# Kernel tuning notes

Hardware: AMD Instinct MI355X
Metric: run time of the kernel (lower is better)

Reference implementation:

```python
import jax, jax.numpy as jnp
import numpy as np

EPS = 1e-5

def layernorm(x, g, b):
    mu = jnp.mean(x, axis=-1, keepdims=True)
    var = jnp.var(x, axis=-1, keepdims=True)
    return (x - mu) * jax.lax.rsqrt(var + EPS) * g + b

def setup_inputs() -> dict:
    B, S, H = 8, 2048, 1024
    key = jax.random.key(0)
    ks = jax.random.split(key, 8)
    lim = 1.0 / np.sqrt(2 * H)  # torch Linear default init scale
    return {
        "input_states": jax.random.normal(ks[0], (B, S, H), jnp.float32),
        "in_g": jnp.ones((H,), jnp.float32), "in_b": jnp.zeros((H,), jnp.float32),
        "st_g": jnp.ones((H,), jnp.float32), "st_b": jnp.zeros((H,), jnp.float32),
        "Wu": jax.random.uniform(ks[1], (H, 2 * H), jnp.float32, -lim, lim),
        "bu": jax.random.uniform(ks[2], (H,), jnp.float32, -lim, lim),
        "Wr": jax.random.uniform(ks[3], (H, 2 * H), jnp.float32, -lim, lim),
        "br": jax.random.uniform(ks[4], (H,), jnp.float32, -lim, lim),
        "Wo": jax.random.uniform(ks[5], (H, 2 * H), jnp.float32, -lim, lim),
        "bo": jax.random.uniform(ks[6], (H,), jnp.float32, -lim, lim),
        "ln_g": jnp.ones((H,), jnp.float32), "ln_b": jnp.zeros((H,), jnp.float32),
    }

def reference(input_states, in_g, in_b, st_g, st_b, Wu, bu, Wr, br, Wo, bo, ln_g, ln_b):
    B, S, H = input_states.shape
    xn = layernorm(input_states, in_g, in_b)            # [B,S,H]
    h0 = jnp.zeros((B, H), input_states.dtype)
    nh0 = layernorm(h0, st_g, st_b)                     # = st_b (zeros input)

    def step(carry, x_t):
        h, nh = carry
        comb = jnp.concatenate([x_t, nh], axis=-1)      # [B,2H]
        u = jax.nn.sigmoid(comb @ Wu.T + bu)
        r = jax.nn.sigmoid(comb @ Wr.T + br)
        comb2 = jnp.concatenate([x_t, r * nh], axis=-1)
        c = jnp.tanh(comb2 @ Wo.T + bo)
        h = (1.0 - u) * h + u * c
        nh = layernorm(h, st_g, st_b)
        return (h, nh), h                               # dropout is identity (eval)

    _, hs = jax.lax.scan(step, (h0, nh0), jnp.swapaxes(xn, 0, 1))  # hs: [S,B,H]
    outputs = jnp.swapaxes(hs, 0, 1)                    # [B,S,H]
    return layernorm(outputs, ln_g, ln_b)
```

## Files before the change

### kernel.cpp

```cpp
#include <hip/hip_runtime.h>


typedef unsigned short bf16_t;
typedef unsigned int u32_t;
typedef u32_t u32x2 __attribute__((ext_vector_type(2)));
typedef u32_t u32x4 __attribute__((ext_vector_type(4)));

__device__ __forceinline__ float bf2f(bf16_t u) {
    return __uint_as_float(((unsigned)u) << 16);
}
__device__ __forceinline__ float bf2f_hi(u32_t d) {
    return __uint_as_float(d & 0xFFFF0000u);
}
__device__ __forceinline__ float bf2f_lo(u32_t d) {
    return __uint_as_float(d << 16);
}
__device__ __forceinline__ bf16_t f2bf(float f) {
    unsigned u = __float_as_uint(f);
    unsigned r = (u + 0x7FFFu + ((u >> 16) & 1u)) >> 16;
    return (bf16_t)r;
}

#define B_  8
#define S_  2048
#define H_  1024
#define EPS 1e-5f
#define NB  512
#define NT  512
#define SENT 0xFFFFu
#define GUARD_MAX 3000000L

template<bool SC1>
__device__ __forceinline__ void tstore(u32_t* p, u32_t v) {
    if (SC1) asm volatile("global_store_dword %0, %1, off sc0 sc1" :: "v"(p), "v"(v) : "memory");
    else     asm volatile("global_store_dword %0, %1, off"          :: "v"(p), "v"(v) : "memory");
}
template<bool SC1>
__device__ __forceinline__ void tstore4(u32_t* p, u32x4 v) {
    if (SC1) asm volatile("global_store_dwordx4 %0, %1, off sc0 sc1" :: "v"(p), "v"(v) : "memory");
    else     asm volatile("global_store_dwordx4 %0, %1, off"          :: "v"(p), "v"(v) : "memory");
}
template<bool SC1>
__device__ __forceinline__ void tload2(u32x2& v, const u32_t* p) {
    if (SC1) asm volatile("global_load_dwordx2 %0, %1, off sc0 sc1" : "=v"(v) : "v"(p));
    else     asm volatile("global_load_dwordx2 %0, %1, off sc0"     : "=v"(v) : "v"(p));
}
template<bool SC1>
__device__ __forceinline__ void tload4(u32x4& v, const u32_t* p) {
    if (SC1) asm volatile("global_load_dwordx4 %0, %1, off sc0 sc1" : "=v"(v) : "v"(p));
    else     asm volatile("global_load_dwordx4 %0, %1, off sc0"     : "=v"(v) : "v"(p));
}
template<bool SC1>
__device__ __forceinline__ u32x2 poll2(const u32_t* p, u32_t tag, long& guard) {
    u32x2 v;
    if (guard > GUARD_MAX) {
        tload2<SC1>(v, p);
        asm volatile("s_waitcnt vmcnt(0)" ::: "memory");
        return v;
    }
    for (;;) {
        tload2<SC1>(v, p);
        asm volatile("s_waitcnt vmcnt(0)" ::: "memory");
        __builtin_amdgcn_sched_barrier(0);
        if ((((v.x ^ tag) | (v.y ^ tag)) & 0xFFFFu) == 0) break;
        __builtin_amdgcn_s_sleep(1);
        if (++guard > GUARD_MAX) break;
    }
    return v;
}

__device__ __forceinline__ float dotp8(u32x4 W, u32x4 X) {
    return bf2f_lo(W.x) * bf2f_lo(X.x) + bf2f_hi(W.x) * bf2f_hi(X.x)
         + bf2f_lo(W.y) * bf2f_lo(X.y) + bf2f_hi(W.y) * bf2f_hi(X.y)
         + bf2f_lo(W.z) * bf2f_lo(X.z) + bf2f_hi(W.z) * bf2f_hi(X.z)
         + bf2f_lo(W.w) * bf2f_lo(X.w) + bf2f_hi(W.w) * bf2f_hi(X.w);
}

__device__ __forceinline__ int rdv(u32_t* cnt, unsigned need, int tid, int* sdead) {
    __syncthreads();
    if (tid == 0) {
        __hip_atomic_fetch_add(cnt, 1u, __ATOMIC_ACQ_REL, __HIP_MEMORY_SCOPE_AGENT);
        long g = 0;
        while (__hip_atomic_load(cnt, __ATOMIC_ACQUIRE, __HIP_MEMORY_SCOPE_AGENT) < need) {
            __builtin_amdgcn_s_sleep(2);
            if (++g > 5000000L) { *sdead = 1; break; }
        }
    }
    __syncthreads();
    return *sdead;
}

__global__ void detect_flag(const unsigned* __restrict__ in_g_bits, int* flag,
                            u32_t* __restrict__ epoch) {
    *flag = (in_g_bits[0] == 0x3F800000u) ? 0 : 1;
    *epoch = *epoch + 1u;
}

__global__ __launch_bounds__(256) void canon_vec(
    const void* v0, const void* v1, const void* v2, const void* v3,
    const void* v4, const void* v5, const void* v6, const void* v7,
    const void* v8, float* __restrict__ dst, const int* __restrict__ flagp)
{
    int isbf = *flagp;
    const void* srcs[9] = {v0, v1, v2, v3, v4, v5, v6, v7, v8};
    const void* s = srcs[blockIdx.y];
    int k = blockIdx.x * 256 + threadIdx.x;
    float val = isbf ? bf2f(((const bf16_t*)s)[k]) : ((const float*)s)[k];
    dst[(long)blockIdx.y * H_ + k] = val;
}

__global__ __launch_bounds__(256) void canon_wh(
    const void* Wu, const void* Wr, const void* Wo,
    bf16_t* __restrict__ Whu, bf16_t* __restrict__ Whr, bf16_t* __restrict__ Who,
    const int* __restrict__ flagp)
{
    int isbf = *flagp;
    const void* srcs[3] = {Wu, Wr, Wo};
    bf16_t* dsts[3] = {Whu, Whr, Who};
    const void* s = srcs[blockIdx.y];
    bf16_t* d = dsts[blockIdx.y];
    long j = blockIdx.x;
#pragma unroll
    for (int i = 0; i < 4; i++) {
        int k = threadIdx.x + i * 256;
        long off = j * (2 * H_) + H_ + k;
        bf16_t v = isbf ? ((const bf16_t*)s)[off] : f2bf(((const float*)s)[off]);
        d[j * H_ + k] = v;
    }
}

__global__ __launch_bounds__(256) void ln_in(
    const void* __restrict__ src, const float* __restrict__ g,
    const float* __restrict__ bt, bf16_t* __restrict__ dst,
    const int* __restrict__ flagp)
{
    int isbf = *flagp;
    long row = blockIdx.x;
    float v[4];
    float s = 0.f, q = 0.f;
#pragma unroll
    for (int i = 0; i < 4; i++) {
        long idx = row * H_ + threadIdx.x + i * 256;
        v[i] = isbf ? bf2f(((const bf16_t*)src)[idx]) : ((const float*)src)[idx];
        s += v[i];
        q += v[i] * v[i];
    }
#pragma unroll
    for (int off = 32; off; off >>= 1) {
        s += __shfl_down(s, off);
        q += __shfl_down(q, off);
    }
    __shared__ float ls[4], lq[4];
    __shared__ float smu, sri;
    int wid = threadIdx.x >> 6, lane = threadIdx.x & 63;
    if (lane == 0) { ls[wid] = s; lq[wid] = q; }
    __syncthreads();
    if (threadIdx.x == 0) {
        float S = ls[0] + ls[1] + ls[2] + ls[3];
        float Q = lq[0] + lq[1] + lq[2] + lq[3];
        float mu = S * (1.f / H_);
        smu = mu;
        sri = rsqrtf(Q * (1.f / H_) - mu * mu + EPS);
    }
    __syncthreads();
    float mu = smu, ri = sri;
#pragma unroll
    for (int i = 0; i < 4; i++) {
        int k = threadIdx.x + i * 256;
        dst[row * H_ + k] = f2bf((v[i] - mu) * ri * g[k] + bt[k]);
    }
}

__global__ __launch_bounds__(256) void ln_out(
    void* __restrict__ buf, const float* __restrict__ g,
    const float* __restrict__ bt, const int* __restrict__ flagp)
{
    int isbf = *flagp;
    long row = blockIdx.x;
    float v[4];
    float s = 0.f, q = 0.f;
#pragma unroll
    for (int i = 0; i < 4; i++) {
        long idx = row * H_ + threadIdx.x + i * 256;
        v[i] = isbf ? bf2f(((const bf16_t*)buf)[idx]) : ((const float*)buf)[idx];
        s += v[i];
        q += v[i] * v[i];
    }
#pragma unroll
    for (int off = 32; off; off >>= 1) {
        s += __shfl_down(s, off);
        q += __shfl_down(q, off);
    }
    __shared__ float ls[4], lq[4];
    __shared__ float smu, sri;
    int wid = threadIdx.x >> 6, lane = threadIdx.x & 63;
    if (lane == 0) { ls[wid] = s; lq[wid] = q; }
    __syncthreads();
    if (threadIdx.x == 0) {
        float S = ls[0] + ls[1] + ls[2] + ls[3];
        float Q = lq[0] + lq[1] + lq[2] + lq[3];
        float mu = S * (1.f / H_);
        smu = mu;
        sri = rsqrtf(Q * (1.f / H_) - mu * mu + EPS);
    }
    __syncthreads();
    float mu = smu, ri = sri;
#pragma unroll
    for (int i = 0; i < 4; i++) {
        long idx = row * H_ + threadIdx.x + i * 256;
        int k = threadIdx.x + i * 256;
        float o = (v[i] - mu) * ri * g[k] + bt[k];
        if (isbf) ((bf16_t*)buf)[idx] = f2bf(o);
        else      ((float*)buf)[idx] = o;
    }
}

__global__ __launch_bounds__(256) void gemm_pre(
    const bf16_t* __restrict__ A,
    const void* __restrict__ Wu, const void* __restrict__ Wr, const void* __restrict__ Wo,
    const float* __restrict__ bias3,
    bf16_t* __restrict__ Pu, bf16_t* __restrict__ Pr, bf16_t* __restrict__ Po,
    const int* __restrict__ flagp)
{
    int isbf = *flagp;
    const void* W;
    const float* bias = bias3 + (long)blockIdx.z * H_;
    bf16_t* C;
    if (blockIdx.z == 0)      { W = Wu; C = Pu; }
    else if (blockIdx.z == 1) { W = Wr; C = Pr; }
    else                      { W = Wo; C = Po; }

    __shared__ float sa[8][128];
    __shared__ float sb[8][128];
    float acc[8][8];
#pragma unroll
    for (int i = 0; i < 8; i++)
#pragma unroll
        for (int j = 0; j < 8; j++) acc[i][j] = 0.f;

    int tx = threadIdx.x % 16, ty = threadIdx.x / 16;
    int m0 = blockIdx.x * 128, n0 = blockIdx.y * 128;
    int lr = threadIdx.x >> 1;
    int lc = (threadIdx.x & 1) * 4;

    for (int kt = 0; kt < H_; kt += 8) {
        ushort4 av = *(const ushort4*)(A + (long)(m0 + lr) * H_ + kt + lc);
        float w0, w1, w2, w3;
        long woff = (long)(n0 + lr) * (2 * H_) + kt + lc;
        if (isbf) {
            ushort4 bv = *(const ushort4*)((const bf16_t*)W + woff);
            w0 = bf2f(bv.x); w1 = bf2f(bv.y); w2 = bf2f(bv.z); w3 = bf2f(bv.w);
        } else {
            float4 bv = *(const float4*)((const float*)W + woff);
            w0 = bv.x; w1 = bv.y; w2 = bv.z; w3 = bv.w;
        }
        sa[lc + 0][lr] = bf2f(av.x); sa[lc + 1][lr] = bf2f(av.y);
        sa[lc + 2][lr] = bf2f(av.z); sa[lc + 3][lr] = bf2f(av.w);
        sb[lc + 0][lr] = w0; sb[lc + 1][lr] = w1;
        sb[lc + 2][lr] = w2; sb[lc + 3][lr] = w3;
        __syncthreads();
#pragma unroll
        for (int k = 0; k < 8; k++) {
            float ar[8], brg[8];
#pragma unroll
            for (int i = 0; i < 8; i++) ar[i] = sa[k][ty * 8 + i];
#pragma unroll
            for (int j = 0; j < 8; j++) brg[j] = sb[k][tx * 8 + j];
#pragma unroll
            for (int i = 0; i < 8; i++)
#pragma unroll
                for (int j = 0; j < 8; j++) acc[i][j] += ar[i] * brg[j];
        }
        __syncthreads();
    }
#pragma unroll
    for (int i = 0; i < 8; i++) {
        long m = m0 + ty * 8 + i;
#pragma unroll
        for (int j = 0; j < 8; j++) {
            int n = n0 + tx * 8 + j;
            C[m * H_ + n] = f2bf(acc[i][j] + bias[n]);
        }
    }
}

template<bool SC1>
__device__ __forceinline__ void scan_loop(
    int b, int j0, int tid, int isbf,
    const bf16_t* __restrict__ Whu, const bf16_t* __restrict__ Whr,
    const bf16_t* __restrict__ Who,
    const bf16_t* __restrict__ Pu, const bf16_t* __restrict__ Pr,
    const bf16_t* __restrict__ Po,
    u32_t* __restrict__ h_tagb, u32_t* __restrict__ rnh_tagb,
    void* __restrict__ outv,
    const float* __restrict__ g_s, const float* __restrict__ bta_s,
    u32_t* __restrict__ hb_s, float* __restrict__ u_s,
    float* __restrict__ ls, float* __restrict__ lq,
    u32_t* __restrict__ rnst, u32_t* __restrict__ hst)
{
    const int w = tid >> 6, l = tid & 63;

    const int dotA  = w * 8 + (l >> 3);
    const int pA    = l & 7;
    const int gate  = dotA >> 5;
    const int colLA = dotA & 31;
    const int colA  = j0 + colLA;
    const bf16_t* WA = gate ? Whr : Whu;
    const bf16_t* PA = gate ? Pr : Pu;
    u32x4 wa[16];
    {
        const u32x4* src = (const u32x4*)(WA + (long)colA * H_ + pA * 128);
#pragma unroll
        for (int i = 0; i < 16; i++) wa[i] = src[i];
    }
    float cb = 0.f, swg = 0.f;
#pragma unroll
    for (int i = 0; i < 16; i++) {
        u32x4 W = wa[i];
        u32_t nw0, nw1, nw2, nw3;
#pragma unroll
        for (int q = 0; q < 4; q++) {
            int k = pA * 128 + i * 8 + q * 2;
            u32_t wq = (q == 0) ? W.x : (q == 1) ? W.y : (q == 2) ? W.z : W.w;
            float w0 = bf2f_lo(wq), w1 = bf2f_hi(wq);
            cb += w0 * bta_s[k] + w1 * bta_s[k + 1];
            bf16_t f0 = f2bf(w0 * g_s[k]);
            bf16_t f1 = f2bf(w1 * g_s[k + 1]);
            swg += bf2f(f0) + bf2f(f1);
            u32_t packed = (u32_t)f0 | ((u32_t)f1 << 16);
            if (q == 0) nw0 = packed; else if (q == 1) nw1 = packed;
            else if (q == 2) nw2 = packed; else nw3 = packed;
        }
        wa[i].x = nw0; wa[i].y = nw1; wa[i].z = nw2; wa[i].w = nw3;
    }
#pragma unroll
    for (int off = 1; off <= 4; off <<= 1) {
        cb  += __shfl_xor(cb, off);
        swg += __shfl_xor(swg, off);
    }

    const int colLB = w * 4 + (l >> 4);
    const int colB  = j0 + colLB;
    const int oB    = l & 15;
    u32x4 wb[8];
    {
        const u32x4* src = (const u32x4*)(Who + (long)colB * H_ + oB * 64);
#pragma unroll
        for (int i = 0; i < 8; i++) wb[i] = src[i];
    }

    const bool ldrA = (pA == 0);
    const bool ldrB = (oB == 0);
    const u32_t* h_pollp  = h_tagb + tid * 2;
    const u32_t* rn_pollp = rnh_tagb + tid * 2;
    const int hoff = w * 68 + (tid & 63);

    float h_reg = 0.f;
    long guard = 0;

    for (int t = 0; t < S_; t++) {
        float pvalA = 0.f, povalB = 0.f;
        if (ldrA) pvalA = bf2f(PA[((long)b * S_ + t) * H_ + colA]);
        if (ldrB) povalB = bf2f(Po[((long)b * S_ + t) * H_ + colB]);

        float x0, x1;
        u32_t hpk;
        if (t == 0) { x0 = 0.f; x1 = 0.f; hpk = 0u; }
        else {
            u32x2 hv = poll2<SC1>(h_pollp, (u32_t)t, guard);
            x0 = bf2f_hi(hv.x); x1 = bf2f_hi(hv.y);
            hpk = (hv.x >> 16) | (hv.y & 0xFFFF0000u);
        }
        hb_s[hoff] = hpk;
        float s = x0 + x1, q = x0 * x0 + x1 * x1;
#pragma unroll
        for (int off = 32; off; off >>= 1) {
            s += __shfl_xor(s, off);
            q += __shfl_xor(q, off);
        }
        if (l == 0) { ls[w] = s; lq[w] = q; }
        __syncthreads();

        float da = 0.f;
        {
            const u32_t* nb = hb_s + pA * 68;
#pragma unroll
            for (int i = 0; i < 16; i++)
                da += dotp8(wa[i], *(const u32x4*)(nb + i * 4));
        }
#pragma unroll
        for (int off = 1; off <= 4; off <<= 1) da += __shfl_xor(da, off);
        if (ldrA) {
            float S = 0.f, Q = 0.f;
#pragma unroll
            for (int i = 0; i < 8; i++) { S += ls[i]; Q += lq[i]; }
            float mu = S * (1.f / H_);
            float ri = rsqrtf(Q * (1.f / H_) - mu * mu + EPS);
            float acc = ri * (da - mu * swg) + cb;
            float sg = 1.f / (1.f + __expf(-(pvalA + acc)));
            if (gate == 0) {
                u_s[colLA] = sg;
            } else {
                u32_t d = hb_s[(colA >> 7) * 68 + ((colA >> 1) & 63)];
                float hj = (colA & 1) ? bf2f_hi(d) : bf2f_lo(d);
                float nhj = (hj - mu) * ri * g_s[colA] + bta_s[colA];
                rnst[colLA] = ((u32_t)f2bf(sg * nhj) << 16) | (u32_t)(t + 1);
            }
        }
        __syncthreads();
        if (tid < 8)
            tstore4<SC1>(rnh_tagb + j0 + tid * 4, *(const u32x4*)(rnst + tid * 4));

        {
            u32x2 rv = poll2<SC1>(rn_pollp, (u32_t)(t + 1), guard);
            hb_s[hoff] = (rv.x >> 16) | (rv.y & 0xFFFF0000u);
        }
        __syncthreads();

        float db = 0.f;
        {
            const u32_t* nb = hb_s + (oB >> 1) * 68 + (oB & 1) * 32;
#pragma unroll
            for (int i = 0; i < 8; i++)
                db += dotp8(wb[i], *(const u32x4*)(nb + i * 4));
        }
#pragma unroll
        for (int off = 1; off <= 8; off <<= 1) db += __shfl_xor(db, off);
        if (ldrB) {
            float c = tanhf(povalB + db);
            float u = u_s[colLB];
            h_reg = h_reg + u * (c - h_reg);
            hst[colLB] = ((u32_t)f2bf(h_reg) << 16) | (u32_t)(t + 1);
            long op = ((long)b * S_ + t) * H_ + colB;
            if (isbf) ((bf16_t*)outv)[op] = f2bf(h_reg);
            else      ((float*)outv)[op]  = h_reg;
        }
        __syncthreads();
        if (tid < 8)
            tstore4<SC1>(h_tagb + j0 + tid * 4, *(const u32x4*)(hst + tid * 4));
    }
}

__global__ __launch_bounds__(NT, 2) void scan_persist(
    const bf16_t* __restrict__ Whu, const bf16_t* __restrict__ Whr,
    const bf16_t* __restrict__ Who,
    const float* __restrict__ st_g, const float* __restrict__ st_b,
    const bf16_t* __restrict__ Pu, const bf16_t* __restrict__ Pr,
    const bf16_t* __restrict__ Po,
    u32_t* __restrict__ h_tag, u32_t* __restrict__ rnh_tag,
    void* __restrict__ outv, const int* __restrict__ flagp,
    const u32_t* __restrict__ epochp,
    u32_t* __restrict__ probe, u32_t* __restrict__ slots,
    u32_t* __restrict__ cnt1, u32_t* __restrict__ cnt2,
    u32_t* __restrict__ slowf)
{
    __shared__ float g_s[H_], bta_s[H_];
    __shared__ u32_t hb_s[8 * 68];
    __shared__ u32_t rnst[32], hst[32];
    __shared__ float u_s[32];
    __shared__ float ls[8], lq[8];
    __shared__ int s_dead, s_tok, s_bad, s_fast, s_batch, s_slot;

    const int tid = threadIdx.x;
    const int isbf = *flagp;
    const u32_t ep = *epochp;
    const u32_t ep2 = ep ^ 0xA5A50000u;
    u32_t* probe2 = probe + 4096;

    __threadfence();

    if (tid == 0) {
        s_dead = 0; s_tok = 0; s_bad = 0; s_fast = 0;
        int x;
        asm volatile("s_getreg_b32 %0, hwreg(HW_REG_XCC_ID)" : "=s"(x));
        x &= 7;
        int batch = -1, slot = 0;
        unsigned s = atomicAdd(&slots[x], 1u);
        if (s < 32u) { batch = x; slot = (int)s; }
        else {
            for (int wt = 0; wt < 40; wt++) __builtin_amdgcn_s_sleep(127);
            for (int k = 1; k <= 8 && batch < 0; k++) {
                int b2 = (x + k) & 7;
                if (__hip_atomic_load(&slots[b2], __ATOMIC_RELAXED,
                                      __HIP_MEMORY_SCOPE_AGENT) < 32u) {
                    unsigned s2 = atomicAdd(&slots[b2], 1u);
                    if (s2 < 32u) { batch = b2; slot = (int)s2; }
                }
            }
        }
        s_batch = batch; s_slot = slot;
    }
    __syncthreads();
    if (s_batch < 0) return;
    const int b = s_batch, j0 = s_slot * 32, slot = s_slot;
    u32_t* h_tagb   = h_tag   + (long)b * H_;
    u32_t* rnh_tagb = rnh_tag + (long)b * H_;

    for (int i = tid; i < H_; i += NT) { g_s[i] = st_g[i]; bta_s[i] = st_b[i]; }

    if (tid < 32) {
        tstore<true>(h_tagb   + j0 + tid, SENT);
        tstore<true>(rnh_tagb + j0 + tid, SENT);
    }
    asm volatile("s_waitcnt vmcnt(0)" ::: "memory");

    if (rdv(cnt1 + b, 32u, tid, &s_dead)) return;

    {
        if (tid == 0) {
            tstore<false>(probe + ((long)b * 32 + slot) * 16, ep);
            asm volatile("s_waitcnt vmcnt(0)" ::: "memory");
        }
        __syncthreads();
        if (tid < 64) {
            const u32_t* pp = probe + ((long)b * 32 + (tid & 31)) * 16;
            bool ok = false;
            long it = 0;
            for (;;) {
                u32_t v;
                asm volatile("global_load_dword %0, %1, off sc0" : "=v"(v) : "v"(pp));
                asm volatile("s_waitcnt vmcnt(0)" ::: "memory");
                __builtin_amdgcn_sched_barrier(0);
                ok = (tid >= 32) || (v == ep);
                if (__ballot(ok) == ~0ull) break;
                __builtin_amdgcn_s_sleep(2);
                if (++it > 20000L) break;
            }
            if (tid == 0) s_tok = (__ballot(ok) == ~0ull) ? 1 : 0;
        }
        __syncthreads();
        if (s_tok) {
            if (tid == 0) {
                tstore<false>(probe2 + ((long)b * 32 + slot) * 16, ep2);
                asm volatile("s_waitcnt vmcnt(0)" ::: "memory");
            }
            __syncthreads();
            if (tid < 64) {
                const u32_t* pp = probe2 + ((long)b * 32 + (tid & 31)) * 16;
                bool ok = false;
                long it = 0;
                for (;;) {
                    u32_t v;
                    asm volatile("global_load_dword %0, %1, off sc0" : "=v"(v) : "v"(pp));
                    asm volatile("s_waitcnt vmcnt(0)" ::: "memory");
                    __builtin_amdgcn_sched_barrier(0);
                    ok = (tid >= 32) || (v == ep2);
                    if (__ballot(ok) == ~0ull) break;
                    __builtin_amdgcn_s_sleep(2);
                    if (++it > 20000L) break;
                }
                if (tid == 0 && __ballot(ok) != ~0ull) s_tok = 0;
            }
        }
    }
    __syncthreads();

    if (s_tok) {
        const u32_t* sp = (tid < 256) ? (h_tagb + tid * 4)
                                      : (rnh_tagb + (tid - 256) * 4);
        u32x4 a;
        tload4<false>(a, sp);
        asm volatile("s_waitcnt vmcnt(0)" ::: "memory");
        __builtin_amdgcn_sched_barrier(0);
        if (a.x != SENT || a.y != SENT || a.z != SENT || a.w != SENT)
            s_bad = 1;
    }
    __syncthreads();

    if (tid == 0) {
        int fastwant = s_tok && !s_bad;
        if (!fastwant)
            __hip_atomic_fetch_add(slowf + b, 1u, __ATOMIC_ACQ_REL,
                                   __HIP_MEMORY_SCOPE_AGENT);
    }
    if (rdv(cnt2 + b, 32u, tid, &s_dead)) return;
    if (tid == 0)
        s_fast = (__hip_atomic_load(slowf + b, __ATOMIC_ACQUIRE,
                                    __HIP_MEMORY_SCOPE_AGENT) == 0u) ? 1 : 0;
    __syncthreads();

    if (s_fast)
        scan_loop<false>(b, j0, tid, isbf, Whu, Whr, Who, Pu, Pr, Po,
                         h_tagb, rnh_tagb, outv, g_s, bta_s, hb_s, u_s,
                         ls, lq, rnst, hst);
    else
        scan_loop<true>(b, j0, tid, isbf, Whu, Whr, Who, Pu, Pr, Po,
                        h_tagb, rnh_tagb, outv, g_s, bta_s, hb_s, u_s,
                        ls, lq, rnst, hst);
}

extern "C" void kernel_launch(void* const* d_in, const int* in_sizes, int n_in,
                              void* d_out, int out_size, void* d_ws, size_t ws_size,
                              hipStream_t stream)
{
    const void* input = d_in[0];
    const void* in_g  = d_in[1];
    const void* in_b  = d_in[2];
    const void* st_g  = d_in[3];
    const void* st_b  = d_in[4];
    const void* Wu    = d_in[5];
    const void* bu    = d_in[6];
    const void* Wr    = d_in[7];
    const void* br    = d_in[8];
    const void* Wo    = d_in[9];
    const void* bo    = d_in[10];
    const void* ln_g  = d_in[11];
    const void* ln_b  = d_in[12];

    const long NTOK = (long)B_ * S_ * H_;

    char* base = (char*)d_ws;
    int*    flag    = (int*)base;
    u32_t*  epoch   = (u32_t*)(base + 64);
    u32_t*  cnt1    = (u32_t*)(base + 512);
    u32_t*  cnt2    = (u32_t*)(base + 640);
    u32_t*  slowf   = (u32_t*)(base + 768);
    u32_t*  slots   = (u32_t*)(base + 896);
    u32_t*  h_tag   = (u32_t*)(base + 4096);
    u32_t*  rnh_tag = h_tag + (long)B_ * H_;
    float*  vecs    = (float*)(rnh_tag + (long)B_ * H_);
    float* c_stg   = vecs + 0 * H_;
    float* c_stb   = vecs + 1 * H_;
    float* c_ing   = vecs + 2 * H_;
    float* c_inb   = vecs + 3 * H_;
    float* c_lng   = vecs + 4 * H_;
    float* c_lnb   = vecs + 5 * H_;
    float* c_bias3 = vecs + 6 * H_;
    bf16_t* Whu = (bf16_t*)(vecs + 9 * H_);
    bf16_t* Whr = Whu + (long)H_ * H_;
    bf16_t* Who = Whr + (long)H_ * H_;
    bf16_t* Pu  = Who + (long)H_ * H_;
    bf16_t* Pr  = Pu + NTOK;
    bf16_t* Po  = Pr + NTOK;
    u32_t*  probe  = (u32_t*)(Po + NTOK);

    bf16_t* xn = (bf16_t*)d_out;

    detect_flag<<<1, 1, 0, stream>>>((const unsigned*)in_g, flag, epoch);

    canon_vec<<<dim3(H_ / 256, 9), 256, 0, stream>>>(
        st_g, st_b, in_g, in_b, ln_g, ln_b, bu, br, bo, vecs, flag);
    canon_wh<<<dim3(H_, 3), 256, 0, stream>>>(Wu, Wr, Wo, Whu, Whr, Who, flag);

    hipMemsetAsync(base + 128, 0, 4096 - 128, stream);

    ln_in<<<B_ * S_, 256, 0, stream>>>(input, c_ing, c_inb, xn, flag);

    gemm_pre<<<dim3(128, 8, 3), 256, 0, stream>>>(
        xn, Wu, Wr, Wo, c_bias3, Pu, Pr, Po, flag);

    scan_persist<<<NB, NT, 0, stream>>>(
        Whu, Whr, Who, c_stg, c_stb, Pu, Pr, Po,
        h_tag, rnh_tag, d_out, flag, epoch, probe, slots, cnt1, cnt2, slowf);

    ln_out<<<B_ * S_, 256, 0, stream>>>(d_out, c_lng, c_lnb, flag);
}
```

Measured before the change: 12.20 ms.

## Publish tagged scan values directly per lane and spread blocks one-per-CU

In the persistent scan, each leader lane now writes its tagged r*nh and h values straight to global memory. Before, these went into shared staging buffers and were flushed as vector stores after a barrier, so the change shortens the critical path of each sequential step. Block-to-batch assignment also claims one CU per XCC through a CAS-owned table, so that two scan blocks of one batch do not share a CU. Timeout guards are lowered. The trade-off is more, smaller global stores per step and an extra memset.

```diff
diff --git a/kernel.cpp b/kernel.cpp
--- a/kernel.cpp
+++ b/kernel.cpp
@@ -28,17 +28,12 @@
 #define NB  512
 #define NT  512
 #define SENT 0xFFFFu
-#define GUARD_MAX 3000000L
+#define GUARD_MAX 2000000L
 
 template<bool SC1>
 __device__ __forceinline__ void tstore(u32_t* p, u32_t v) {
     if (SC1) asm volatile("global_store_dword %0, %1, off sc0 sc1" :: "v"(p), "v"(v) : "memory");
     else     asm volatile("global_store_dword %0, %1, off"          :: "v"(p), "v"(v) : "memory");
-}
-template<bool SC1>
-__device__ __forceinline__ void tstore4(u32_t* p, u32x4 v) {
-    if (SC1) asm volatile("global_store_dwordx4 %0, %1, off sc0 sc1" :: "v"(p), "v"(v) : "memory");
-    else     asm volatile("global_store_dwordx4 %0, %1, off"          :: "v"(p), "v"(v) : "memory");
 }
 template<bool SC1>
 __device__ __forceinline__ void tload2(u32x2& v, const u32_t* p) {
@@ -83,7 +78,7 @@
         long g = 0;
         while (__hip_atomic_load(cnt, __ATOMIC_ACQUIRE, __HIP_MEMORY_SCOPE_AGENT) < need) {
             __builtin_amdgcn_s_sleep(2);
-            if (++g > 5000000L) { *sdead = 1; break; }
+            if (++g > 3000000L) { *sdead = 1; break; }
         }
     }
     __syncthreads();
@@ -295,8 +290,7 @@
     void* __restrict__ outv,
     const float* __restrict__ g_s, const float* __restrict__ bta_s,
     u32_t* __restrict__ hb_s, float* __restrict__ u_s,
-    float* __restrict__ ls, float* __restrict__ lq,
-    u32_t* __restrict__ rnst, u32_t* __restrict__ hst)
+    float* __restrict__ ls, float* __restrict__ lq)
 {
     const int w = tid >> 6, l = tid & 63;
 
@@ -351,6 +345,8 @@
 
     const bool ldrA = (pA == 0);
     const bool ldrB = (oB == 0);
+    u32_t* rn_my = rnh_tagb + colA;
+    u32_t* h_my  = h_tagb + colB;
     const u32_t* h_pollp  = h_tagb + tid * 2;
     const u32_t* rn_pollp = rnh_tagb + tid * 2;
     const int hoff = w * 68 + (tid & 63);
@@ -404,12 +400,10 @@
                 u32_t d = hb_s[(colA >> 7) * 68 + ((colA >> 1) & 63)];
                 float hj = (colA & 1) ? bf2f_hi(d) : bf2f_lo(d);
                 float nhj = (hj - mu) * ri * g_s[colA] + bta_s[colA];
-                rnst[colLA] = ((u32_t)f2bf(sg * nhj) << 16) | (u32_t)(t + 1);
+                tstore<SC1>(rn_my, ((u32_t)f2bf(sg * nhj) << 16) | (u32_t)(t + 1));
             }
         }
         __syncthreads();
-        if (tid < 8)
-            tstore4<SC1>(rnh_tagb + j0 + tid * 4, *(const u32x4*)(rnst + tid * 4));
 
         {
             u32x2 rv = poll2<SC1>(rn_pollp, (u32_t)(t + 1), guard);
@@ -430,14 +424,12 @@
             float c = tanhf(povalB + db);
             float u = u_s[colLB];
             h_reg = h_reg + u * (c - h_reg);
-            hst[colLB] = ((u32_t)f2bf(h_reg) << 16) | (u32_t)(t + 1);
+            tstore<SC1>(h_my, ((u32_t)f2bf(h_reg) << 16) | (u32_t)(t + 1));
             long op = ((long)b * S_ + t) * H_ + colB;
             if (isbf) ((bf16_t*)outv)[op] = f2bf(h_reg);
             else      ((float*)outv)[op]  = h_reg;
         }
         __syncthreads();
-        if (tid < 8)
-            tstore4<SC1>(h_tagb + j0 + tid * 4, *(const u32x4*)(hst + tid * 4));
     }
 }
 
@@ -452,11 +444,10 @@
     const u32_t* __restrict__ epochp,
     u32_t* __restrict__ probe, u32_t* __restrict__ slots,
     u32_t* __restrict__ cnt1, u32_t* __restrict__ cnt2,
-    u32_t* __restrict__ slowf)
+    u32_t* __restrict__ slowf, u32_t* __restrict__ cuown)
 {
     __shared__ float g_s[H_], bta_s[H_];
     __shared__ u32_t hb_s[8 * 68];
-    __shared__ u32_t rnst[32], hst[32];
     __shared__ float u_s[32];
     __shared__ float ls[8], lq[8];
     __shared__ int s_dead, s_tok, s_bad, s_fast, s_batch, s_slot;
@@ -474,12 +465,17 @@
         int x;
         asm volatile("s_getreg_b32 %0, hwreg(HW_REG_XCC_ID)" : "=s"(x));
         x &= 7;
+        unsigned hwid;
+        asm volatile("s_getreg_b32 %0, hwreg(HW_REG_HW_ID)" : "=s"(hwid));
+        unsigned cukey = (hwid >> 8) & 0xFFu;
         int batch = -1, slot = 0;
-        unsigned s = atomicAdd(&slots[x], 1u);
-        if (s < 32u) { batch = x; slot = (int)s; }
-        else {
+        if (atomicCAS(&cuown[x * 256 + cukey], 0u, 1u) == 0u) {
+            unsigned s = atomicAdd(&slots[x], 1u);
+            if (s < 32u) { batch = x; slot = (int)s; }
+        }
+        if (batch < 0) {
             for (int wt = 0; wt < 40; wt++) __builtin_amdgcn_s_sleep(127);
-            for (int k = 1; k <= 8 && batch < 0; k++) {
+            for (int k = 0; k < 8 && batch < 0; k++) {
                 int b2 = (x + k) & 7;
                 if (__hip_atomic_load(&slots[b2], __ATOMIC_RELAXED,
                                       __HIP_MEMORY_SCOPE_AGENT) < 32u) {
@@ -581,12 +577,10 @@
 
     if (s_fast)
         scan_loop<false>(b, j0, tid, isbf, Whu, Whr, Who, Pu, Pr, Po,
-                         h_tagb, rnh_tagb, outv, g_s, bta_s, hb_s, u_s,
-                         ls, lq, rnst, hst);
+                         h_tagb, rnh_tagb, outv, g_s, bta_s, hb_s, u_s, ls, lq);
     else
         scan_loop<true>(b, j0, tid, isbf, Whu, Whr, Who, Pu, Pr, Po,
-                        h_tagb, rnh_tagb, outv, g_s, bta_s, hb_s, u_s,
-                        ls, lq, rnst, hst);
+                        h_tagb, rnh_tagb, outv, g_s, bta_s, hb_s, u_s, ls, lq);
 }
 
 extern "C" void kernel_launch(void* const* d_in, const int* in_sizes, int n_in,
@@ -632,7 +626,8 @@
     bf16_t* Pu  = Who + (long)H_ * H_;
     bf16_t* Pr  = Pu + NTOK;
     bf16_t* Po  = Pr + NTOK;
-    u32_t*  probe  = (u32_t*)(Po + NTOK);
+    u32_t*  probe = (u32_t*)(Po + NTOK);
+    u32_t*  cuown = probe + 8192;
 
     bf16_t* xn = (bf16_t*)d_out;
 
@@ -643,6 +638,7 @@
     canon_wh<<<dim3(H_, 3), 256, 0, stream>>>(Wu, Wr, Wo, Whu, Whr, Who, flag);
 
     hipMemsetAsync(base + 128, 0, 4096 - 128, stream);
+    hipMemsetAsync(cuown, 0, 8 * 256 * sizeof(u32_t), stream);
 
     ln_in<<<B_ * S_, 256, 0, stream>>>(input, c_ing, c_inb, xn, flag);
 
@@ -651,7 +647,8 @@
 
     scan_persist<<<NB, NT, 0, stream>>>(
         Whu, Whr, Who, c_stg, c_stb, Pu, Pr, Po,
-        h_tag, rnh_tag, d_out, flag, epoch, probe, slots, cnt1, cnt2, slowf);
+        h_tag, rnh_tag, d_out, flag, epoch, probe, slots, cnt1, cnt2,
+        slowf, cuown);
 
     ln_out<<<B_ * S_, 256, 0, stream>>>(d_out, c_lng, c_lnb, flag);
 }
```

After: 11.69 ms. 4.1% less time.
